# Optimization experiments

Measured on AMD Instinct MI355X. Metric: run time of the kernel, lower is better.

Reference implementation:

```python
import jax, jax.numpy as jnp
import numpy as np

RADIUS = 3
DIAM = 2 * RADIUS + 1  # 7 -> 49 taps
KEY_DIM = 32
GN_GROUPS = 32
GN_EPS = 1e-5

_WE = [-0.03515625, 0.26171875, 0.87890625, -0.10546875]  # even outputs (frac 0.75)
_WO = [-0.10546875, 0.87890625, 0.26171875, -0.03515625]  # odd outputs (frac 0.25)


def _up2x_axis(x, axis):
    """2x bicubic upsample (a=-0.75, half-pixel, edge-clamped) along one axis."""
    pads = [(2, 2) if i == axis else (0, 0) for i in range(x.ndim)]
    xp = jnp.pad(x, pads, mode='edge')
    n = x.shape[axis]

    def sl(o):
        idx = [slice(None)] * x.ndim
        idx[axis] = slice(o, o + n)
        return xp[tuple(idx)]

    even = sum(_WE[j] * sl(j) for j in range(4))
    odd = sum(_WO[j] * sl(j + 1) for j in range(4))
    out = jnp.stack([even, odd], axis=axis + 1)
    shp = list(x.shape)
    shp[axis] = 2 * n
    return out.reshape(shp)


def bicubic_up2x(x):
    return _up2x_axis(_up2x_axis(x, 2), 3)


def conv1x1(x, w, b=None):
    # x: [B,C,H,W], w: [O,C]
    y = jnp.einsum('bchw,oc->bohw', x, w)
    if b is not None:
        y = y + b[None, :, None, None]
    return y


def jbu_step(source, guidance, rp_w1, rp_b1, rp_w2, rp_b2, temp, sigma):
    """One x2 JBULearnedRange step. source: [B,C,h,w], guidance: full-res [B,3,H0,W0]."""
    B, C, h, w = source.shape
    H, W = 2 * h, 2 * w
    g = jax.image.resize(guidance, (B, guidance.shape[1], H, W), method='linear')
    g = g.astype(source.dtype)

    # learned range projection (1x1 conv -> GELU -> 1x1 conv); dropout is eval identity
    proj = conv1x1(g, rp_w1, rp_b1)
    proj = jax.nn.gelu(proj, approximate=False)
    proj = conv1x1(proj, rp_w2, rp_b2)  # [B,K,H,W]

    pp = jnp.pad(proj, ((0, 0), (0, 0), (RADIUS, RADIUS), (RADIUS, RADIUS)), mode='reflect')
    # per-shift center<->neighbor similarity, shift order = row-major (dy outer, dx inner)
    sims = jnp.stack([jnp.sum(pp[:, :, dy:dy + H, dx:dx + W] * proj, axis=1)
                      for dy in range(DIAM) for dx in range(DIAM)], axis=1)  # [B,P,H,W]
    t = jnp.clip(jnp.exp(temp), 1e-4, 1e4)
    range_kernel = jax.nn.softmax(t * sims, axis=1)

    dist = jnp.linspace(-1.0, 1.0, DIAM)
    spatial = jnp.exp(-(dist[:, None] ** 2 + dist[None, :] ** 2) / (2.0 * sigma ** 2))
    spatial = spatial.reshape(1, DIAM * DIAM, 1, 1)

    ck = range_kernel * spatial
    ck = ck / jnp.clip(jnp.sum(ck, axis=1, keepdims=True), 1e-7, None)

    hr = bicubic_up2x(source)  # [B,C,H,W]
    hp = jnp.pad(hr, ((0, 0), (0, 0), (RADIUS, RADIUS), (RADIUS, RADIUS)), mode='reflect')
    out = jnp.zeros_like(hr)
    p = 0
    for dy in range(DIAM):
        for dx in range(DIAM):
            out = out + ck[:, p:p + 1] * hp[:, :, dy:dy + H, dx:dx + W]
            p += 1
    return out


def group_norm(x, w, b):
    B, C, H, W = x.shape
    xg = x.reshape(B, GN_GROUPS, C // GN_GROUPS, H, W)
    m = xg.mean(axis=(2, 3, 4), keepdims=True)
    v = jnp.mean((xg - m) ** 2, axis=(2, 3, 4), keepdims=True)
    xg = (xg - m) * jax.lax.rsqrt(v + GN_EPS)
    return xg.reshape(B, C, H, W) * w[None, :, None, None] + b[None, :, None, None]


def setup_inputs() -> dict:
    key = jax.random.key(0)
    ks = jax.random.split(key, 16)
    B, FD, MD, OD = 2, 384, 256, 256
    h, w = 48, 80
    inp = {
        'source': jax.random.normal(ks[0], (B, FD, h, w), dtype=jnp.float32),
        'guidance': jax.random.uniform(ks[1], (B, 3, 16 * h, 16 * w), dtype=jnp.float32),
        'pre_proj_w': jax.random.normal(ks[2], (MD, FD), dtype=jnp.float32) / np.sqrt(FD),
        'rp1_w1': jax.random.normal(ks[3], (KEY_DIM, 3), dtype=jnp.float32) / np.sqrt(3.0),
        'rp1_b1': jnp.zeros((KEY_DIM,), jnp.float32),
        'rp1_w2': jax.random.normal(ks[4], (KEY_DIM, KEY_DIM), dtype=jnp.float32) / np.sqrt(KEY_DIM),
        'rp1_b2': jnp.zeros((KEY_DIM,), jnp.float32),
        'temp1': jnp.asarray(0.0, jnp.float32),
        'sigma1': jnp.asarray(1.0, jnp.float32),
        'rp2_w1': jax.random.normal(ks[5], (KEY_DIM, 3), dtype=jnp.float32) / np.sqrt(3.0),
        'rp2_b1': jnp.zeros((KEY_DIM,), jnp.float32),
        'rp2_w2': jax.random.normal(ks[6], (KEY_DIM, KEY_DIM), dtype=jnp.float32) / np.sqrt(KEY_DIM),
        'rp2_b2': jnp.zeros((KEY_DIM,), jnp.float32),
        'temp2': jnp.asarray(0.0, jnp.float32),
        'sigma2': jnp.asarray(1.0, jnp.float32),
        'fixup_w': jax.random.normal(ks[7], (MD, MD), dtype=jnp.float32) / np.sqrt(MD),
        'gn_w': jnp.ones((MD,), jnp.float32),
        'gn_b': jnp.zeros((MD,), jnp.float32),
        'proj_w': jax.random.normal(ks[8], (OD, MD), dtype=jnp.float32) / np.sqrt(MD),
    }
    return inp


def reference(source, guidance, pre_proj_w,
              rp1_w1, rp1_b1, rp1_w2, rp1_b2, temp1, sigma1,
              rp2_w1, rp2_b1, rp2_w2, rp2_b2, temp2, sigma2,
              fixup_w, gn_w, gn_b, proj_w):
    x = conv1x1(source, pre_proj_w)
    x = jbu_step(x, guidance, rp1_w1, rp1_b1, rp1_w2, rp1_b2, temp1, sigma1)  # H/16 -> H/8
    x = jbu_step(x, guidance, rp2_w1, rp2_b1, rp2_w2, rp2_b2, temp2, sigma2)  # H/8 -> H/4
    x = x + 0.1 * conv1x1(x, fixup_w)  # FixUp residual (Dropout2d is eval identity)
    x = group_norm(x, gn_w, gn_b)
    return conv1x1(x, proj_w)
```

## Files before the change

kernel.cpp:

```cpp
#include <hip/hip_runtime.h>
#include <math.h>

#define B_ 2
#define C_ 256
#define FD_ 384
#define K_ 32
#define HW2 61440

typedef __attribute__((ext_vector_type(8))) short s8b;
typedef __attribute__((ext_vector_type(16))) float fvec16;
typedef __attribute__((ext_vector_type(4))) float f4;

__device__ __forceinline__ unsigned short f2bf(float f) {
    unsigned int u = __builtin_bit_cast(unsigned int, f);
    u = (u + 0x7fffu + ((u >> 16) & 1u)) >> 16;
    return (unsigned short)u;
}

__global__ void k_preproj(const float* __restrict__ src, const float* __restrict__ w,
                          float* __restrict__ out) {
    __shared__ float w_s[2 * FD_];
    int bo = blockIdx.x;
    int b = bo >> 7, o = (bo & 127) * 2;
    int tid = threadIdx.x;
    for (int i = tid; i < 2 * FD_; i += 256) w_s[i] = w[o * FD_ + i];
    __syncthreads();
    float a0[15], a1[15];
#pragma unroll
    for (int k = 0; k < 15; k++) { a0[k] = 0.f; a1[k] = 0.f; }
    const float* sp = src + (long)b * FD_ * 3840;
    for (int c = 0; c < FD_; c++) {
        float wv0 = w_s[c];
        float wv1 = w_s[FD_ + c];
        const float* row = sp + (long)c * 3840;
#pragma unroll
        for (int k = 0; k < 15; k++) {
            float r = row[tid + k * 256];
            a0[k] += wv0 * r;
            a1[k] += wv1 * r;
        }
    }
    float* op = out + ((long)b * 256 + o) * 3840;
#pragma unroll
    for (int k = 0; k < 15; k++) op[tid + k * 256] = a0[k];
#pragma unroll
    for (int k = 0; k < 15; k++) op[3840 + tid + k * 256] = a1[k];
}

__global__ void k_down_h(const float* __restrict__ in, float* __restrict__ out, int Ho, float s) {
    long idx = (long)blockIdx.x * 256 + threadIdx.x;
    long total = (long)B_ * 3 * Ho * 1280;
    if (idx >= total) return;
    int x = (int)(idx % 1280);
    long t1 = idx / 1280;
    int i = (int)(t1 % Ho);
    long t2 = t1 / Ho;
    int c = (int)(t2 % 3);
    int b = (int)(t2 / 3);
    float sf = (i + 0.5f) * s - 0.5f;
    int j0 = (int)floorf(sf - s) + 1;
    int j1 = (int)ceilf(sf + s) - 1;
    float acc = 0.f, wsum = 0.f;
    const float* ip = in + ((long)(b * 3 + c) * 768) * 1280 + x;
    for (int j = j0; j <= j1; j++) {
        if (j < 0 || j >= 768) continue;
        float wv = 1.f - fabsf((float)j - sf) / s;
        acc += wv * ip[(long)j * 1280];
        wsum += wv;
    }
    out[idx] = acc / wsum;
}

__global__ void k_down_w(const float* __restrict__ in, float* __restrict__ out, int Ho, int Wo, float s) {
    long idx = (long)blockIdx.x * 256 + threadIdx.x;
    long total = (long)B_ * 3 * Ho * Wo;
    if (idx >= total) return;
    int i = (int)(idx % Wo);
    long t1 = idx / Wo;
    int y = (int)(t1 % Ho);
    long t2 = t1 / Ho;
    int c = (int)(t2 % 3);
    int b = (int)(t2 / 3);
    float sf = (i + 0.5f) * s - 0.5f;
    int j0 = (int)floorf(sf - s) + 1;
    int j1 = (int)ceilf(sf + s) - 1;
    float acc = 0.f, wsum = 0.f;
    const float* ip = in + ((long)(b * 3 + c) * Ho + y) * 1280;
    for (int j = j0; j <= j1; j++) {
        if (j < 0 || j >= 1280) continue;
        float wv = 1.f - fabsf((float)j - sf) / s;
        acc += wv * ip[j];
        wsum += wv;
    }
    out[idx] = acc / wsum;
}

__global__ void k_proj(const float* __restrict__ g, float* __restrict__ proj,
                       const float* __restrict__ w1, const float* __restrict__ b1,
                       const float* __restrict__ w2, const float* __restrict__ b2,
                       int HW) {
    __shared__ float w1_s[96], b1_s[32], w2_s[1024], b2_s[32];
    int tid = threadIdx.x;
    if (tid < 96) w1_s[tid] = w1[tid];
    if (tid < 32) { b1_s[tid] = b1[tid]; b2_s[tid] = b2[tid]; }
    for (int i = tid; i < 1024; i += 256) w2_s[i] = w2[i];
    __syncthreads();
    long idx = (long)blockIdx.x * 256 + tid;
    if (idx >= (long)B_ * HW) return;
    int b = (int)(idx / HW);
    int pix = (int)(idx % HW);
    const float* gp = g + (long)b * 3 * HW + pix;
    float g0 = gp[0], g1 = gp[HW], g2 = gp[2 * (long)HW];
    float hg[32];
#pragma unroll
    for (int k = 0; k < 32; k++) {
        float h = b1_s[k] + w1_s[k * 3] * g0 + w1_s[k * 3 + 1] * g1 + w1_s[k * 3 + 2] * g2;
        hg[k] = 0.5f * h * (1.f + erff(h * 0.70710678118654752f));
    }
    float* pp = proj + (long)b * 32 * HW + pix;
#pragma unroll
    for (int j = 0; j < 32; j++) {
        float a = b2_s[j];
#pragma unroll
        for (int k = 0; k < 32; k++) a += w2_s[j * 32 + k] * hg[k];
        pp[(long)j * HW] = a;
    }
}

__global__ __launch_bounds__(256) void k_ck(const float* __restrict__ proj,
                                            float* __restrict__ ckb,
                                            const float* __restrict__ temp,
                                            const float* __restrict__ sigma,
                                            int H, int W) {
    __shared__ __align__(16) float smem[9680];

    int tid = threadIdx.x;
    int tx = tid & 15, ty = tid >> 4;
    int x0 = blockIdx.x * 16, y0 = blockIdx.y * 16;
    int b = blockIdx.z;

    float ck[49];
#pragma unroll
    for (int p = 0; p < 49; p++) ck[p] = 0.f;

    const float* pb = proj + (long)b * 32 * H * W;
    const f4* hs4 = (const f4*)smem;
#pragma unroll 1
    for (int pass = 0; pass < 2; pass++) {
        int k0 = pass * 16;
        for (int i = tid; i < 16 * 484; i += 256) {
            int k = i / 484;
            int rem = i - k * 484;
            int yy = rem / 22, xx = rem - yy * 22;
            int y = y0 - 3 + yy; y = y < 0 ? -y : (y >= H ? 2 * H - 2 - y : y);
            int x = x0 - 3 + xx; x = x < 0 ? -x : (x >= W ? 2 * W - 2 - x : x);
            smem[rem * 20 + k] = pb[((long)(k0 + k) * H + y) * W + x];
        }
        __syncthreads();
        int pc = ((ty + 3) * 22 + (tx + 3)) * 5;
        f4 c0 = hs4[pc + 0], c1 = hs4[pc + 1], c2 = hs4[pc + 2], c3 = hs4[pc + 3];
#pragma unroll
        for (int dy = 0; dy < 7; dy++) {
#pragma unroll
            for (int dx = 0; dx < 7; dx++) {
                int pn = ((ty + dy) * 22 + (tx + dx)) * 5;
                f4 s = hs4[pn + 0] * c0;
                s += hs4[pn + 1] * c1;
                s += hs4[pn + 2] * c2;
                s += hs4[pn + 3] * c3;
                ck[dy * 7 + dx] += (s.x + s.y) + (s.z + s.w);
            }
        }
        __syncthreads();
    }

    {
        float t = expf(temp[0]);
        t = fminf(fmaxf(t, 1e-4f), 1e4f);
        float m = -1e30f;
#pragma unroll
        for (int p = 0; p < 49; p++) { ck[p] *= t; m = fmaxf(m, ck[p]); }
        float ssum = 0.f;
#pragma unroll
        for (int p = 0; p < 49; p++) { ck[p] = expf(ck[p] - m); ssum += ck[p]; }
        float inv = 1.f / ssum;
        float sg = sigma[0];
        float dc = 1.f / (2.f * sg * sg);
        float csum = 0.f;
#pragma unroll
        for (int p = 0; p < 49; p++) {
            int dy = p / 7, dx = p % 7;
            float d0 = (dy - 3) / 3.f, d1 = (dx - 3) / 3.f;
            float sp = expf(-(d0 * d0 + d1 * d1) * dc);
            ck[p] = ck[p] * inv * sp;
            csum += ck[p];
        }
        float r = 1.f / fmaxf(csum, 1e-7f);
#pragma unroll
        for (int p = 0; p < 49; p++) ck[p] *= r;
    }

    long HWl = (long)H * W;
    float* cp = ckb + (long)b * 49 * HWl + (long)(y0 + ty) * W + (x0 + tx);
#pragma unroll
    for (int p = 0; p < 49; p++) cp[(long)p * HWl] = ck[p];
}

template <int CS>
__global__ __launch_bounds__(256) void k_apply(const float* __restrict__ lo,
                                               const float* ckb,
                                               float* out,
                                               int H, int W, int h, int w) {
    __shared__ __align__(16) float smem[8952];

    int tid = threadIdx.x;
    int tx = tid & 15, ty = tid >> 4;
    int x0 = blockIdx.x * 16, y0 = blockIdx.y * 16;
    int b = blockIdx.z / CS;
    int c_base = (blockIdx.z % CS) * (256 / CS);

    int HW = H * W;
    const float* cp = ckb + (long)b * 49 * HW + (y0 + ty) * W + (x0 + tx);

    int ws_y = y0 - 3; if (ws_y < 0) ws_y = 0; if (ws_y > H - 22) ws_y = H - 22;
    int ws_x = x0 - 3; if (ws_x < 0) ws_x = 0; if (ws_x > W - 22) ws_x = W - 22;
    int ls_y = (ws_y >> 1) - 2, ls_x = (ws_x >> 1) - 2;
    int ry[7], rx[7];
#pragma unroll
    for (int d = 0; d < 7; d++) {
        int v = y0 + ty + d - 3; v = v < 0 ? -v : (v >= H ? 2 * H - 2 - v : v);
        ry[d] = (v - ws_y) * 45;
        int u = x0 + tx + d - 3; u = u < 0 ? -u : (u >= W ? 2 * W - 2 - u : u);
        rx[d] = (u - ws_x) * 2;
    }

    int lrow = ls_y + ty; lrow = lrow < 0 ? 0 : (lrow >= h ? h - 1 : lrow);
    int lcol = ls_x + tx; lcol = lcol < 0 ? 0 : (lcol >= w ? w - 1 : lcol);

    f4* lo4  = (f4*)smem;
    f4* tmp4 = (f4*)(smem + 2112);
    f4* hr4  = (f4*)(smem + 2112 + 2880);

    int hw = h * w;

    const int nchunk = (256 / CS) / 8;
#pragma unroll 1
    for (int cc = 0; cc < nchunk; cc++) {
        int c0 = c_base + cc * 8;
        const float* lp = lo + ((long)(b * 256 + c0) * h + lrow) * w + lcol;
        {
            f4 va;
            va.x = lp[0];      va.y = lp[hw];     va.z = lp[2 * hw]; va.w = lp[3 * hw];
            lo4[ty * 33 + tx * 2 + 0] = va;
        }
        {
            f4 vb;
            vb.x = lp[4 * hw]; vb.y = lp[5 * hw]; vb.z = lp[6 * hw]; vb.w = lp[7 * hw];
            lo4[ty * 33 + tx * 2 + 1] = vb;
        }
        __syncthreads();

#pragma unroll
        for (int it = 0; it < 3; it++) {
            int e = tid + it * 256;
            if (e < 704) {
                int g = e & 1, rem = e >> 1;
                int j = rem / 22, Xp = rem - j * 22;
                int X = ws_x + Xp;
                int ix = (X >> 1) - ls_x;
                const f4* lr = lo4 + j * 33 + g;
                f4 v;
                if (X & 1)
                    v = -0.10546875f * lr[(ix - 1) * 2] + 0.87890625f * lr[ix * 2] + 0.26171875f * lr[(ix + 1) * 2] - 0.03515625f * lr[(ix + 2) * 2];
                else
                    v = -0.03515625f * lr[(ix - 2) * 2] + 0.26171875f * lr[(ix - 1) * 2] + 0.87890625f * lr[ix * 2] - 0.10546875f * lr[(ix + 1) * 2];
                tmp4[j * 45 + Xp * 2 + g] = v;
            }
        }
        __syncthreads();

#pragma unroll
        for (int it = 0; it < 4; it++) {
            int e = tid + it * 256;
            if (e < 968) {
                int g = e & 1, rem = e >> 1;
                int i = rem / 22, Xp = rem - i * 22;
                int Y = ws_y + i;
                int jy = (Y >> 1) - ls_y;
                const f4* tc = tmp4 + Xp * 2 + g;
                f4 v;
                if (Y & 1)
                    v = -0.10546875f * tc[(jy - 1) * 45] + 0.87890625f * tc[jy * 45] + 0.26171875f * tc[(jy + 1) * 45] - 0.03515625f * tc[(jy + 2) * 45];
                else
                    v = -0.03515625f * tc[(jy - 2) * 45] + 0.26171875f * tc[(jy - 1) * 45] + 0.87890625f * tc[jy * 45] - 0.10546875f * tc[(jy + 1) * 45];
                hr4[i * 45 + Xp * 2 + g] = v;
            }
        }
        __syncthreads();

        f4 acc0 = (f4)(0.f), acc1 = (f4)(0.f);
#pragma unroll
        for (int dy = 0; dy < 7; dy++) {
            float c_[7];
            int cko = dy * 7 * HW;
#pragma unroll
            for (int dx = 0; dx < 7; dx++) c_[dx] = cp[cko + dx * HW];
            const f4* hrow = hr4 + ry[dy];
#pragma unroll
            for (int dx = 0; dx < 7; dx++) {
                acc0 += c_[dx] * hrow[rx[dx]];
                acc1 += c_[dx] * hrow[rx[dx] + 1];
            }
        }
        float* op = out + ((long)(b * 256 + c0) * H + (y0 + ty)) * W + (x0 + tx);
        op[0]          = acc0.x;
        op[HW]         = acc0.y;
        op[2 * HW]     = acc0.z;
        op[3 * HW]     = acc0.w;
        op[4 * HW]     = acc1.x;
        op[5 * HW]     = acc1.y;
        op[6 * HW]     = acc1.z;
        op[7 * HW]     = acc1.w;
    }
}

__global__ void k_prepw(const float* __restrict__ w, unsigned short* __restrict__ wf) {
    int blk = blockIdx.x;
    int lane = threadIdx.x;
    int mt = blk >> 4, ks = blk & 15;
    int o = mt * 32 + (lane & 31);
    int c = ks * 16 + (lane >> 5) * 8;
    const float* wp = w + (long)o * 256 + c;
    float4 v0 = *(const float4*)wp;
    float4 v1 = *(const float4*)(wp + 4);
    unsigned short* dst = wf + ((long)(blk * 64 + lane)) * 8;
    unsigned int r0 = f2bf(v0.x) | ((unsigned int)f2bf(v0.y) << 16);
    unsigned int r1 = f2bf(v0.z) | ((unsigned int)f2bf(v0.w) << 16);
    unsigned int r2 = f2bf(v1.x) | ((unsigned int)f2bf(v1.y) << 16);
    unsigned int r3 = f2bf(v1.z) | ((unsigned int)f2bf(v1.w) << 16);
    uint4 pk = {r0, r1, r2, r3};
    *(uint4*)dst = pk;
}

#define LDK 264
template <bool GN, bool RESID>
__global__ __launch_bounds__(256) void k_gemm256(float* __restrict__ x,
                                                 const unsigned short* __restrict__ wf,
                                                 const float* __restrict__ stats,
                                                 const float* __restrict__ gn_w,
                                                 const float* __restrict__ gn_b,
                                                 float* __restrict__ part) {
    __shared__ unsigned short xs[64 * LDK];
    __shared__ float scl_s[256], sh_s[256];
    __shared__ float gs[64];
    int tid = threadIdx.x;
    int b = blockIdx.y;
    int pix0 = blockIdx.x * 64;
    float* xb = x + (long)b * 256 * HW2;

    if (RESID && tid < 64) gs[tid] = 0.f;

    if (GN) {
        int c = tid;
        int g = c >> 3;
        float mean = stats[(b * 32 + g) * 2];
        float rstd = stats[(b * 32 + g) * 2 + 1];
        float s = rstd * gn_w[c];
        scl_s[c] = s;
        sh_s[c] = gn_b[c] - mean * s;
        __syncthreads();
    }

#pragma unroll
    for (int it = 0; it < 4; it++) {
        int c0 = ((tid >> 4) << 2) + it * 64;
        int px = (tid & 15) << 2;
        const float* gp = xb + (long)c0 * HW2 + pix0 + px;
        float4 v0 = *(const float4*)gp;
        float4 v1 = *(const float4*)(gp + HW2);
        float4 v2 = *(const float4*)(gp + 2 * HW2);
        float4 v3 = *(const float4*)(gp + 3 * HW2);
        if (GN) {
            float s0 = scl_s[c0], h0 = sh_s[c0];
            float s1 = scl_s[c0 + 1], h1 = sh_s[c0 + 1];
            float s2 = scl_s[c0 + 2], h2 = sh_s[c0 + 2];
            float s3 = scl_s[c0 + 3], h3 = sh_s[c0 + 3];
            v0.x = v0.x * s0 + h0; v0.y = v0.y * s0 + h0; v0.z = v0.z * s0 + h0; v0.w = v0.w * s0 + h0;
            v1.x = v1.x * s1 + h1; v1.y = v1.y * s1 + h1; v1.z = v1.z * s1 + h1; v1.w = v1.w * s1 + h1;
            v2.x = v2.x * s2 + h2; v2.y = v2.y * s2 + h2; v2.z = v2.z * s2 + h2; v2.w = v2.w * s2 + h2;
            v3.x = v3.x * s3 + h3; v3.y = v3.y * s3 + h3; v3.z = v3.z * s3 + h3; v3.w = v3.w * s3 + h3;
        }
        float p0[4] = {v0.x, v0.y, v0.z, v0.w};
        float p1[4] = {v1.x, v1.y, v1.z, v1.w};
        float p2[4] = {v2.x, v2.y, v2.z, v2.w};
        float p3[4] = {v3.x, v3.y, v3.z, v3.w};
#pragma unroll
        for (int p = 0; p < 4; p++) {
            ushort4 u;
            u.x = f2bf(p0[p]); u.y = f2bf(p1[p]); u.z = f2bf(p2[p]); u.w = f2bf(p3[p]);
            *(ushort4*)&xs[(px + p) * LDK + c0] = u;
        }
    }
    __syncthreads();

    int lane = tid & 63, wv = tid >> 6;
    fvec16 acc[2][2];
#pragma unroll
    for (int mi = 0; mi < 2; mi++)
#pragma unroll
        for (int ni = 0; ni < 2; ni++)
            acc[mi][ni] = (fvec16)(0.f);

    int n_in = lane & 31;
    int koff = (lane >> 5) * 8;
#pragma unroll
    for (int ks = 0; ks < 16; ks++) {
        s8b a0 = *(const s8b*)(wf + ((long)(((wv * 2 + 0) * 16 + ks) * 64 + lane)) * 8);
        s8b a1 = *(const s8b*)(wf + ((long)(((wv * 2 + 1) * 16 + ks) * 64 + lane)) * 8);
        s8b b0 = *(const s8b*)&xs[(0 + n_in) * LDK + ks * 16 + koff];
        s8b b1 = *(const s8b*)&xs[(32 + n_in) * LDK + ks * 16 + koff];
        acc[0][0] = __builtin_amdgcn_mfma_f32_32x32x16_bf16(a0, b0, acc[0][0], 0, 0, 0);
        acc[0][1] = __builtin_amdgcn_mfma_f32_32x32x16_bf16(a0, b1, acc[0][1], 0, 0, 0);
        acc[1][0] = __builtin_amdgcn_mfma_f32_32x32x16_bf16(a1, b0, acc[1][0], 0, 0, 0);
        acc[1][1] = __builtin_amdgcn_mfma_f32_32x32x16_bf16(a1, b1, acc[1][1], 0, 0, 0);
    }

    int hh = lane >> 5;
    float ls[2][4], lq[2][4];
    if (RESID) {
#pragma unroll
        for (int mi = 0; mi < 2; mi++)
#pragma unroll
            for (int gq = 0; gq < 4; gq++) { ls[mi][gq] = 0.f; lq[mi][gq] = 0.f; }
    }
#pragma unroll
    for (int mi = 0; mi < 2; mi++) {
        int mt = wv * 2 + mi;
#pragma unroll
        for (int ni = 0; ni < 2; ni++) {
            int pix = pix0 + ni * 32 + n_in;
#pragma unroll
            for (int r = 0; r < 16; r++) {
                int row = (r & 3) + 8 * (r >> 2) + 4 * hh;
                long addr = (long)(mt * 32 + row) * HW2 + pix;
                if (RESID) {
                    float v = xb[addr] + 0.1f * acc[mi][ni][r];
                    xb[addr] = v;
                    ls[mi][r >> 2] += v;
                    lq[mi][r >> 2] += v * v;
                } else {
                    xb[addr] = acc[mi][ni][r];
                }
            }
        }
    }
    if (RESID) {
#pragma unroll
        for (int mi = 0; mi < 2; mi++)
#pragma unroll
            for (int gq = 0; gq < 4; gq++) {
                int g = (wv * 2 + mi) * 4 + gq;
                atomicAdd(&gs[g * 2], ls[mi][gq]);
                atomicAdd(&gs[g * 2 + 1], lq[mi][gq]);
            }
        __syncthreads();
        if (tid < 64) {
            int g = tid >> 1, which = tid & 1;
            part[((long)(b * 32 + g) * 960 + blockIdx.x) * 2 + which] = gs[tid];
        }
    }
}

__global__ void k_gnred2(const float* __restrict__ part, float* __restrict__ stats) {
    __shared__ double s_s[256], q_s[256];
    int t = blockIdx.x;
    const float* p = part + (long)t * 960 * 2;
    double s = 0.0, q = 0.0;
    for (int i = threadIdx.x; i < 960; i += 256) {
        s += p[2 * i];
        q += p[2 * i + 1];
    }
    s_s[threadIdx.x] = s; q_s[threadIdx.x] = q;
    __syncthreads();
    for (int st = 128; st > 0; st >>= 1) {
        if (threadIdx.x < st) { s_s[threadIdx.x] += s_s[threadIdx.x + st]; q_s[threadIdx.x] += q_s[threadIdx.x + st]; }
        __syncthreads();
    }
    if (threadIdx.x == 0) {
        double N = 8.0 * HW2;
        double mean = s_s[0] / N;
        double var = q_s[0] / N - mean * mean;
        stats[t * 2] = (float)mean;
        stats[t * 2 + 1] = (float)(1.0 / sqrt(var + 1e-5));
    }
}

extern "C" void kernel_launch(void* const* d_in, const int* in_sizes, int n_in,
                              void* d_out, int out_size, void* d_ws, size_t ws_size,
                              hipStream_t stream) {
    const float* src      = (const float*)d_in[0];
    const float* guidance = (const float*)d_in[1];
    const float* pre_w    = (const float*)d_in[2];
    const float* rp1_w1   = (const float*)d_in[3];
    const float* rp1_b1   = (const float*)d_in[4];
    const float* rp1_w2   = (const float*)d_in[5];
    const float* rp1_b2   = (const float*)d_in[6];
    const float* temp1    = (const float*)d_in[7];
    const float* sigma1   = (const float*)d_in[8];
    const float* rp2_w1   = (const float*)d_in[9];
    const float* rp2_b1   = (const float*)d_in[10];
    const float* rp2_w2   = (const float*)d_in[11];
    const float* rp2_b2   = (const float*)d_in[12];
    const float* temp2    = (const float*)d_in[13];
    const float* sigma2   = (const float*)d_in[14];
    const float* fixup_w  = (const float*)d_in[15];
    const float* gn_w     = (const float*)d_in[16];
    const float* gn_b     = (const float*)d_in[17];
    const float* proj_w   = (const float*)d_in[18];
    float* out = (float*)d_out;

    char* ws = (char*)d_ws;
    size_t off = 0;
    auto alloc = [&](size_t bytes) { size_t o = off; off = (off + bytes + 255) & ~(size_t)255; return o; };
    float* gdown  = (float*)(ws + alloc((size_t)2 * 3 * 192 * 1280 * 4));
    float* gbuf   = (float*)(ws + alloc((size_t)2 * 3 * 192 * 320 * 4));
    float* projb  = (float*)(ws + alloc((size_t)2 * 32 * 192 * 320 * 4));
    float* x1     = (float*)(ws + alloc((size_t)2 * 256 * 48 * 80 * 4));
    float* out1   = (float*)(ws + alloc((size_t)2 * 256 * 96 * 160 * 4));
    float* ckbuf  = (float*)(ws + alloc((size_t)2 * 49 * 192 * 320 * 4));
    unsigned short* wfFix  = (unsigned short*)(ws + alloc(65536 * 2));
    unsigned short* wfProj = (unsigned short*)(ws + alloc(65536 * 2));
    float* gpart  = (float*)(ws + alloc((size_t)64 * 960 * 2 * 4));
    float* stats  = (float*)(ws + alloc(64 * 2 * 4));

    k_prepw<<<128, 64, 0, stream>>>(fixup_w, wfFix);
    k_prepw<<<128, 64, 0, stream>>>(proj_w, wfProj);

    k_preproj<<<256, 256, 0, stream>>>(src, pre_w, x1);

    {
        const int H = 96, W = 160, HW = H * W;
        k_down_h<<<(2 * 3 * H * 1280) / 256, 256, 0, stream>>>(guidance, gdown, H, 8.f);
        k_down_w<<<(2 * 3 * HW + 255) / 256, 256, 0, stream>>>(gdown, gbuf, H, W, 8.f);
        k_proj<<<(2 * HW + 255) / 256, 256, 0, stream>>>(gbuf, projb, rp1_w1, rp1_b1, rp1_w2, rp1_b2, HW);
        k_ck<<<dim3(W / 16, H / 16, 2), 256, 0, stream>>>(projb, ckbuf, temp1, sigma1, H, W);
        k_apply<4><<<dim3(W / 16, H / 16, 2 * 4), 256, 0, stream>>>(x1, ckbuf, out1, H, W, 48, 80);
    }

    {
        const int H = 192, W = 320, HW = H * W;
        k_down_h<<<(2 * 3 * H * 1280) / 256, 256, 0, stream>>>(guidance, gdown, H, 4.f);
        k_down_w<<<(2 * 3 * HW + 255) / 256, 256, 0, stream>>>(gdown, gbuf, H, W, 4.f);
        k_proj<<<(2 * HW + 255) / 256, 256, 0, stream>>>(gbuf, projb, rp2_w1, rp2_b1, rp2_w2, rp2_b2, HW);
        k_ck<<<dim3(W / 16, H / 16, 2), 256, 0, stream>>>(projb, ckbuf, temp2, sigma2, H, W);
        k_apply<4><<<dim3(W / 16, H / 16, 2 * 4), 256, 0, stream>>>(out1, ckbuf, out, H, W, 96, 160);
    }

    k_gemm256<false, true><<<dim3(960, 2), 256, 0, stream>>>(out, wfFix, nullptr, nullptr, nullptr, gpart);
    k_gnred2<<<64, 256, 0, stream>>>(gpart, stats);
    k_gemm256<true, false><<<dim3(960, 2), 256, 0, stream>>>(out, wfProj, stats, gn_w, gn_b, nullptr);
}
```

Before: 892.6 us.

## Widen k_apply tile to 32x16 with two pixels per thread and split channels 8-way

Each thread in the JBU apply kernel now computes two horizontally adjacent output pixels. The tile widens to 32 columns, and the 8 shared-memory high-res neighbor vectors per row are reused across both pixels' 7 taps. The shared-memory layout is reorganized into planar halves (the g*24, g*39 strides), and the low-res load becomes a cooperative loop. Channel splitting goes from 4 to 8 to keep the grid size up. The aim is to cut LDS reads and amortize the bicubic upsample halo per output, at the cost of more shared memory per block (about 60KB), which may lower occupancy, and non-coalesced stride-2 reads of the combined-kernel buffer.

```diff
diff --git a/kernel.cpp b/kernel.cpp
--- a/kernel.cpp
+++ b/kernel.cpp
@@ -211,35 +211,37 @@
                                                const float* ckb,
                                                float* out,
                                                int H, int W, int h, int w) {
-    __shared__ __align__(16) float smem[8952];
+    __shared__ __align__(16) float smem[14928];
 
     int tid = threadIdx.x;
     int tx = tid & 15, ty = tid >> 4;
-    int x0 = blockIdx.x * 16, y0 = blockIdx.y * 16;
+    int x0 = blockIdx.x * 32, y0 = blockIdx.y * 16;
     int b = blockIdx.z / CS;
     int c_base = (blockIdx.z % CS) * (256 / CS);
 
     int HW = H * W;
-    const float* cp = ckb + (long)b * 49 * HW + (y0 + ty) * W + (x0 + tx);
+    int xp = x0 + 2 * tx;
+    const float* cp = ckb + (long)b * 49 * HW + (y0 + ty) * W + xp;
 
     int ws_y = y0 - 3; if (ws_y < 0) ws_y = 0; if (ws_y > H - 22) ws_y = H - 22;
-    int ws_x = x0 - 3; if (ws_x < 0) ws_x = 0; if (ws_x > W - 22) ws_x = W - 22;
+    int ws_x = x0 - 3; if (ws_x < 0) ws_x = 0; if (ws_x > W - 38) ws_x = W - 38;
     int ls_y = (ws_y >> 1) - 2, ls_x = (ws_x >> 1) - 2;
-    int ry[7], rx[7];
+    int ry[7];
 #pragma unroll
     for (int d = 0; d < 7; d++) {
         int v = y0 + ty + d - 3; v = v < 0 ? -v : (v >= H ? 2 * H - 2 - v : v);
-        ry[d] = (v - ws_y) * 45;
-        int u = x0 + tx + d - 3; u = u < 0 ? -u : (u >= W ? 2 * W - 2 - u : u);
-        rx[d] = (u - ws_x) * 2;
-    }
-
-    int lrow = ls_y + ty; lrow = lrow < 0 ? 0 : (lrow >= h ? h - 1 : lrow);
-    int lcol = ls_x + tx; lcol = lcol < 0 ? 0 : (lcol >= w ? w - 1 : lcol);
+        ry[d] = (v - ws_y) * 78;
+    }
+    int rxu[8];
+#pragma unroll
+    for (int d = 0; d < 8; d++) {
+        int u = xp + d - 3; u = u < 0 ? -u : (u >= W ? 2 * W - 2 - u : u);
+        rxu[d] = u - ws_x;
+    }
 
     f4* lo4  = (f4*)smem;
-    f4* tmp4 = (f4*)(smem + 2112);
-    f4* hr4  = (f4*)(smem + 2112 + 2880);
+    f4* tmp4 = ((f4*)smem) + 768;
+    f4* hr4  = ((f4*)smem) + 2016;
 
     int hw = h * w;
 
@@ -247,80 +249,106 @@
 #pragma unroll 1
     for (int cc = 0; cc < nchunk; cc++) {
         int c0 = c_base + cc * 8;
-        const float* lp = lo + ((long)(b * 256 + c0) * h + lrow) * w + lcol;
-        {
-            f4 va;
-            va.x = lp[0];      va.y = lp[hw];     va.z = lp[2 * hw]; va.w = lp[3 * hw];
-            lo4[ty * 33 + tx * 2 + 0] = va;
-        }
-        {
-            f4 vb;
-            vb.x = lp[4 * hw]; vb.y = lp[5 * hw]; vb.z = lp[6 * hw]; vb.w = lp[7 * hw];
-            lo4[ty * 33 + tx * 2 + 1] = vb;
-        }
-        __syncthreads();
-
-#pragma unroll
-        for (int it = 0; it < 3; it++) {
+        const float* lpb = lo + (long)(b * 256 + c0) * hw;
+#pragma unroll
+        for (int it = 0; it < 2; it++) {
             int e = tid + it * 256;
-            if (e < 704) {
+            if (e < 368) {
+                int r = e / 23, c = e - r * 23;
+                int lr = ls_y + r; lr = lr < 0 ? 0 : (lr >= h ? h - 1 : lr);
+                int lc = ls_x + c; lc = lc < 0 ? 0 : (lc >= w ? w - 1 : lc);
+                const float* lp = lpb + lr * w + lc;
+                f4 va;
+                va.x = lp[0];      va.y = lp[hw];     va.z = lp[2 * hw]; va.w = lp[3 * hw];
+                lo4[r * 48 + c] = va;
+                f4 vb;
+                vb.x = lp[4 * hw]; vb.y = lp[5 * hw]; vb.z = lp[6 * hw]; vb.w = lp[7 * hw];
+                lo4[r * 48 + 24 + c] = vb;
+            }
+        }
+        __syncthreads();
+
+#pragma unroll
+        for (int it = 0; it < 5; it++) {
+            int e = tid + it * 256;
+            if (e < 1216) {
                 int g = e & 1, rem = e >> 1;
-                int j = rem / 22, Xp = rem - j * 22;
+                int j = rem / 38, Xp = rem - j * 38;
                 int X = ws_x + Xp;
                 int ix = (X >> 1) - ls_x;
-                const f4* lr = lo4 + j * 33 + g;
+                const f4* lr = lo4 + j * 48 + g * 24;
                 f4 v;
                 if (X & 1)
-                    v = -0.10546875f * lr[(ix - 1) * 2] + 0.87890625f * lr[ix * 2] + 0.26171875f * lr[(ix + 1) * 2] - 0.03515625f * lr[(ix + 2) * 2];
+                    v = -0.10546875f * lr[ix - 1] + 0.87890625f * lr[ix] + 0.26171875f * lr[ix + 1] - 0.03515625f * lr[ix + 2];
                 else
-                    v = -0.03515625f * lr[(ix - 2) * 2] + 0.26171875f * lr[(ix - 1) * 2] + 0.87890625f * lr[ix * 2] - 0.10546875f * lr[(ix + 1) * 2];
-                tmp4[j * 45 + Xp * 2 + g] = v;
-            }
-        }
-        __syncthreads();
-
-#pragma unroll
-        for (int it = 0; it < 4; it++) {
+                    v = -0.03515625f * lr[ix - 2] + 0.26171875f * lr[ix - 1] + 0.87890625f * lr[ix] - 0.10546875f * lr[ix + 1];
+                tmp4[j * 78 + g * 39 + Xp] = v;
+            }
+        }
+        __syncthreads();
+
+#pragma unroll
+        for (int it = 0; it < 7; it++) {
             int e = tid + it * 256;
-            if (e < 968) {
+            if (e < 1672) {
                 int g = e & 1, rem = e >> 1;
-                int i = rem / 22, Xp = rem - i * 22;
+                int i = rem / 38, Xp = rem - i * 38;
                 int Y = ws_y + i;
                 int jy = (Y >> 1) - ls_y;
-                const f4* tc = tmp4 + Xp * 2 + g;
+                const f4* tc = tmp4 + g * 39 + Xp;
                 f4 v;
                 if (Y & 1)
-                    v = -0.10546875f * tc[(jy - 1) * 45] + 0.87890625f * tc[jy * 45] + 0.26171875f * tc[(jy + 1) * 45] - 0.03515625f * tc[(jy + 2) * 45];
+                    v = -0.10546875f * tc[(jy - 1) * 78] + 0.87890625f * tc[jy * 78] + 0.26171875f * tc[(jy + 1) * 78] - 0.03515625f * tc[(jy + 2) * 78];
                 else
-                    v = -0.03515625f * tc[(jy - 2) * 45] + 0.26171875f * tc[(jy - 1) * 45] + 0.87890625f * tc[jy * 45] - 0.10546875f * tc[(jy + 1) * 45];
-                hr4[i * 45 + Xp * 2 + g] = v;
-            }
-        }
-        __syncthreads();
-
-        f4 acc0 = (f4)(0.f), acc1 = (f4)(0.f);
+                    v = -0.03515625f * tc[(jy - 2) * 78] + 0.26171875f * tc[(jy - 1) * 78] + 0.87890625f * tc[jy * 78] - 0.10546875f * tc[(jy + 1) * 78];
+                hr4[i * 78 + g * 39 + Xp] = v;
+            }
+        }
+        __syncthreads();
+
+        f4 a00 = (f4)(0.f), a01 = (f4)(0.f);
+        f4 a10 = (f4)(0.f), a11 = (f4)(0.f);
 #pragma unroll
         for (int dy = 0; dy < 7; dy++) {
-            float c_[7];
+            float c0_[7], c1_[7];
             int cko = dy * 7 * HW;
 #pragma unroll
-            for (int dx = 0; dx < 7; dx++) c_[dx] = cp[cko + dx * HW];
+            for (int dx = 0; dx < 7; dx++) {
+                c0_[dx] = cp[cko + dx * HW];
+                c1_[dx] = cp[cko + dx * HW + 1];
+            }
             const f4* hrow = hr4 + ry[dy];
+            f4 h0[8], h1[8];
+#pragma unroll
+            for (int d = 0; d < 8; d++) {
+                h0[d] = hrow[rxu[d]];
+                h1[d] = hrow[39 + rxu[d]];
+            }
 #pragma unroll
             for (int dx = 0; dx < 7; dx++) {
-                acc0 += c_[dx] * hrow[rx[dx]];
-                acc1 += c_[dx] * hrow[rx[dx] + 1];
-            }
-        }
-        float* op = out + ((long)(b * 256 + c0) * H + (y0 + ty)) * W + (x0 + tx);
-        op[0]          = acc0.x;
-        op[HW]         = acc0.y;
-        op[2 * HW]     = acc0.z;
-        op[3 * HW]     = acc0.w;
-        op[4 * HW]     = acc1.x;
-        op[5 * HW]     = acc1.y;
-        op[6 * HW]     = acc1.z;
-        op[7 * HW]     = acc1.w;
+                a00 += c0_[dx] * h0[dx];
+                a01 += c0_[dx] * h1[dx];
+                a10 += c1_[dx] * h0[dx + 1];
+                a11 += c1_[dx] * h1[dx + 1];
+            }
+        }
+        float* op = out + ((long)(b * 256 + c0) * H + (y0 + ty)) * W + xp;
+        op[0]          = a00.x;
+        op[HW]         = a00.y;
+        op[2 * HW]     = a00.z;
+        op[3 * HW]     = a00.w;
+        op[4 * HW]     = a01.x;
+        op[5 * HW]     = a01.y;
+        op[6 * HW]     = a01.z;
+        op[7 * HW]     = a01.w;
+        op[1]          = a10.x;
+        op[HW + 1]     = a10.y;
+        op[2 * HW + 1] = a10.z;
+        op[3 * HW + 1] = a10.w;
+        op[4 * HW + 1] = a11.x;
+        op[5 * HW + 1] = a11.y;
+        op[6 * HW + 1] = a11.z;
+        op[7 * HW + 1] = a11.w;
     }
 }
 
@@ -544,7 +572,7 @@
         k_down_w<<<(2 * 3 * HW + 255) / 256, 256, 0, stream>>>(gdown, gbuf, H, W, 8.f);
         k_proj<<<(2 * HW + 255) / 256, 256, 0, stream>>>(gbuf, projb, rp1_w1, rp1_b1, rp1_w2, rp1_b2, HW);
         k_ck<<<dim3(W / 16, H / 16, 2), 256, 0, stream>>>(projb, ckbuf, temp1, sigma1, H, W);
-        k_apply<4><<<dim3(W / 16, H / 16, 2 * 4), 256, 0, stream>>>(x1, ckbuf, out1, H, W, 48, 80);
+        k_apply<8><<<dim3(W / 32, H / 16, 2 * 8), 256, 0, stream>>>(x1, ckbuf, out1, H, W, 48, 80);
     }
 
     {
@@ -553,7 +581,7 @@
         k_down_w<<<(2 * 3 * HW + 255) / 256, 256, 0, stream>>>(gdown, gbuf, H, W, 4.f);
         k_proj<<<(2 * HW + 255) / 256, 256, 0, stream>>>(gbuf, projb, rp2_w1, rp2_b1, rp2_w2, rp2_b2, HW);
         k_ck<<<dim3(W / 16, H / 16, 2), 256, 0, stream>>>(projb, ckbuf, temp2, sigma2, H, W);
-        k_apply<4><<<dim3(W / 16, H / 16, 2 * 4), 256, 0, stream>>>(out1, ckbuf, out, H, W, 96, 160);
+        k_apply<8><<<dim3(W / 32, H / 16, 2 * 8), 256, 0, stream>>>(out1, ckbuf, out, H, W, 96, 160);
     }
 
     k_gemm256<false, true><<<dim3(960, 2), 256, 0, stream>>>(out, wfFix, nullptr, nullptr, nullptr, gpart);
```

New measurement: 865.1 us. 1.03x faster.
